# Optimization experiments

Hardware: AMD Instinct MI355X
Metric: run time of the kernel (lower is better)

## Reference

```python
import jax, jax.numpy as jnp
import numpy as np

EPS = 1e-5

def _ln(x, g, b):
    m = jnp.mean(x, -1, keepdims=True)
    v = jnp.var(x, -1, keepdims=True)
    return (x - m) / jnp.sqrt(v + EPS) * g + b

def _rel_shift(x):
    # x: [B, qlen, klen, n_head] -- TransformerXL relative shift
    b, q, k, n = x.shape
    xp = jnp.pad(x, ((0, 0), (0, 0), (1, 0), (0, 0)))  # zero-pad along klen front
    xp = xp.reshape(b, k + 1, q, n)[:, 1:]
    return xp.reshape(b, q, k, n)

def setup_inputs() -> dict:
    key = jax.random.key(0)
    B, Q, D, N, DH, DI = 4, 1024, 1024, 16, 64, 4096
    ks = jax.random.split(key, 9)
    s = 0.02
    w = jax.random.normal(ks[0], (B, Q, D), jnp.float32)
    r = jax.random.normal(ks[1], (1, Q, D), jnp.float32)
    attention_mask = jnp.triu(jnp.ones((Q, Q), bool), k=1)  # 1 == masked (causal)
    qkv_w = jax.random.normal(ks[2], (3 * D, D), jnp.float32) * s
    r_w = jax.random.normal(ks[3], (D, D), jnp.float32) * s
    o_w = jax.random.normal(ks[4], (D, D), jnp.float32) * s
    r_w_bias = jax.random.normal(ks[5], (N, DH), jnp.float32) * s
    r_r_bias = jax.random.normal(ks[6], (N, DH), jnp.float32) * s
    ln1_g = jnp.ones(D, jnp.float32); ln1_b = jnp.zeros(D, jnp.float32)
    ff_w1 = jax.random.normal(ks[7], (DI, D), jnp.float32) * s
    ff_b1 = jnp.zeros(DI, jnp.float32)
    ff_w2 = jax.random.normal(ks[8], (D, DI), jnp.float32) * s
    ff_b2 = jnp.zeros(D, jnp.float32)
    ln2_g = jnp.ones(D, jnp.float32); ln2_b = jnp.zeros(D, jnp.float32)
    return dict(w=w, r=r, attention_mask=attention_mask, qkv_w=qkv_w, r_w=r_w,
                o_w=o_w, r_w_bias=r_w_bias, r_r_bias=r_r_bias, ln1_g=ln1_g,
                ln1_b=ln1_b, ff_w1=ff_w1, ff_b1=ff_b1, ff_w2=ff_w2, ff_b2=ff_b2,
                ln2_g=ln2_g, ln2_b=ln2_b)

def reference(w, r, attention_mask, qkv_w, r_w, o_w, r_w_bias, r_r_bias,
              ln1_g, ln1_b, ff_w1, ff_b1, ff_w2, ff_b2, ln2_g, ln2_b):
    B, Q, D = w.shape
    N, DH = r_w_bias.shape
    # QKV projection (post-lnorm path, no mem)
    heads = w @ qkv_w.T  # [B,Q,3D]
    q, k, v = jnp.split(heads, 3, axis=-1)
    q = q.reshape(B, Q, N, DH)
    k = k.reshape(B, Q, N, DH)
    v = v.reshape(B, Q, N, DH)
    rk = (r[0] @ r_w.T).reshape(Q, N, DH)  # [rlen,N,DH]
    # content (AC) and position (BD) terms, computed in fp32 as in original
    AC = jnp.einsum('bind,bjnd->bijn', q + r_w_bias, k)
    BD = _rel_shift(jnp.einsum('bind,jnd->bijn', q + r_r_bias, rk))
    score = (AC + BD) * (1.0 / jnp.sqrt(jnp.float32(DH)))
    score = jnp.where(attention_mask[None, :, :, None], -1e30, score)
    prob = jax.nn.softmax(score, axis=2)  # softmax over klen
    av = jnp.einsum('bijn,bjnd->bind', prob, v).reshape(B, Q, D)
    out1 = _ln(w + av @ o_w.T, ln1_g, ln1_b)  # deepnorm_alpha = 1.0
    ff = jax.nn.relu(out1 @ ff_w1.T + ff_b1) @ ff_w2.T + ff_b2
    return _ln(out1 + ff, ln2_g, ln2_b)
```

## Files before the change

kernel.cpp:

```cpp
#include <hip/hip_runtime.h>
#include <hip/hip_bf16.h>

typedef __attribute__((ext_vector_type(8))) short short8;
typedef __attribute__((ext_vector_type(4))) short short4v;
typedef __attribute__((ext_vector_type(4))) float floatx4;

__device__ inline float bs2f(short s) {
    unsigned int u = ((unsigned int)(unsigned short)s) << 16;
    float f; __builtin_memcpy(&f, &u, 4); return f;
}
__device__ inline short f2bs(float f) {
    __hip_bfloat16 h = __float2bfloat16(f);
    unsigned short u; __builtin_memcpy(&u, &h, 2); return (short)u;
}
__device__ inline float ldf(const float* p)           { return *p; }
__device__ inline float ldf(const __hip_bfloat16* p)  { return __bfloat162float(*p); }
__device__ inline void  stf(float* p, float v)          { *p = v; }
__device__ inline void  stf(__hip_bfloat16* p, float v) { *p = __float2bfloat16(v); }

__device__ inline void gl_lds16(const short* g, short* l) {
    __builtin_amdgcn_global_load_lds(
        (const __attribute__((address_space(1))) void*)g,
        (__attribute__((address_space(3))) void*)l, 16, 0, 0);
}

__global__ __launch_bounds__(256) void f2b_all_kernel(
    const float* __restrict__ s0, const float* __restrict__ s1,
    const float* __restrict__ s2, const float* __restrict__ s3,
    const float* __restrict__ s4, const float* __restrict__ s5,
    const float* __restrict__ s6, __hip_bfloat16* __restrict__ dst)
{
    const long id  = blockIdx.x;
    const long gid = id * 1024 + threadIdx.x * 4;
    const float* src; long base;
    if      (id < 4096)  { src = s0; base = 0; }
    else if (id < 5120)  { src = s1; base = 4096L  * 1024; }
    else if (id < 8192)  { src = s2; base = 5120L  * 1024; }
    else if (id < 9216)  { src = s3; base = 8192L  * 1024; }
    else if (id < 10240) { src = s4; base = 9216L  * 1024; }
    else if (id < 14336) { src = s5; base = 10240L * 1024; }
    else                 { src = s6; base = 14336L * 1024; }
    const float4 v = *(const float4*)(src + (gid - base));
    dst[gid + 0] = __float2bfloat16(v.x);
    dst[gid + 1] = __float2bfloat16(v.y);
    dst[gid + 2] = __float2bfloat16(v.z);
    dst[gid + 3] = __float2bfloat16(v.w);
}

__global__ __launch_bounds__(256, 2) void gemm128_nt_kernel(
    const __hip_bfloat16* __restrict__ A,
    const __hip_bfloat16* __restrict__ Bw,
    __hip_bfloat16* __restrict__ C,
    int M, int N, int K,
    const float* __restrict__ bias,
    int do_relu)
{
    __shared__ short lA[128 * 32];
    __shared__ short lB[128 * 32];

    const int lane = threadIdx.x & 63;
    const int w    = threadIdx.x >> 6;
    const int m16  = lane & 15;
    const int quad = lane >> 4;
    const int wr   = w >> 1, wc = w & 1;

    const long i0 = (long)blockIdx.y * 128;
    const long j0 = (long)blockIdx.x * 128;

    const short* Ap = (const short*)A;
    const short* Bp = (const short*)Bw;

    floatx4 acc[4][4];
    #pragma unroll
    for (int a = 0; a < 4; ++a)
        #pragma unroll
        for (int b = 0; b < 4; ++b) acc[a][b] = (floatx4){0.f, 0.f, 0.f, 0.f};

    const int srow = w * 32 + (lane >> 2);
    const int scol = (lane & 3) * 8;
    const short* ga = Ap + (i0 + srow) * K + scol;
    const short* gb = Bp + (j0 + srow) * K + scol;
    short* la = lA + (w * 32) * 32;
    short* lb = lB + (w * 32) * 32;

    for (int k0 = 0; k0 < K; k0 += 32) {
        __syncthreads();
        gl_lds16(ga + k0,            la);
        gl_lds16(ga + 16 * K + k0,   la + 16 * 32);
        gl_lds16(gb + k0,            lb);
        gl_lds16(gb + 16 * K + k0,   lb + 16 * 32);
        __syncthreads();

        short8 af[4], bf[4];
        #pragma unroll
        for (int rb = 0; rb < 4; ++rb)
            af[rb] = *(const short8*)&lA[(wr * 64 + rb * 16 + m16) * 32 + quad * 8];
        #pragma unroll
        for (int cb = 0; cb < 4; ++cb)
            bf[cb] = *(const short8*)&lB[(wc * 64 + cb * 16 + m16) * 32 + quad * 8];
        #pragma unroll
        for (int rb = 0; rb < 4; ++rb)
            #pragma unroll
            for (int cb = 0; cb < 4; ++cb)
                acc[rb][cb] = __builtin_amdgcn_mfma_f32_16x16x32_bf16(
                    af[rb], bf[cb], acc[rb][cb], 0, 0, 0);
    }

    #pragma unroll
    for (int cb = 0; cb < 4; ++cb) {
        const long j = j0 + wc * 64 + cb * 16 + m16;
        const float bv = bias ? bias[j] : 0.f;
        #pragma unroll
        for (int rb = 0; rb < 4; ++rb) {
            #pragma unroll
            for (int rr = 0; rr < 4; ++rr) {
                const long row = i0 + wr * 64 + rb * 16 + quad * 4 + rr;
                float v = acc[rb][cb][rr] + bv;
                if (do_relu) v = fmaxf(v, 0.f);
                C[row * N + j] = __float2bfloat16(v);
            }
        }
    }
}

__global__ __launch_bounds__(256, 2) void gemm_n64_nt_kernel(
    const __hip_bfloat16* __restrict__ A,
    const __hip_bfloat16* __restrict__ Bw,
    __hip_bfloat16* __restrict__ C,
    int M, int N, int K,
    const float* __restrict__ bias,
    int do_relu)
{
    __shared__ short lA[128 * 32];
    __shared__ short lB[64 * 32];

    const int lane = threadIdx.x & 63;
    const int w    = threadIdx.x >> 6;
    const int m16  = lane & 15;
    const int quad = lane >> 4;
    const int wr   = w >> 1, wc = w & 1;

    const long i0 = (long)blockIdx.y * 128;
    const long j0 = (long)blockIdx.x * 64;

    const short* Ap = (const short*)A;
    const short* Bp = (const short*)Bw;

    floatx4 acc[4][2];
    #pragma unroll
    for (int a = 0; a < 4; ++a)
        #pragma unroll
        for (int b = 0; b < 2; ++b) acc[a][b] = (floatx4){0.f, 0.f, 0.f, 0.f};

    const int srowA = w * 32 + (lane >> 2);
    const int srowB = w * 16 + (lane >> 2);
    const int scol  = (lane & 3) * 8;
    const short* ga = Ap + (i0 + srowA) * K + scol;
    const short* gb = Bp + (j0 + srowB) * K + scol;
    short* la = lA + (w * 32) * 32;
    short* lb = lB + (w * 16) * 32;

    for (int k0 = 0; k0 < K; k0 += 32) {
        __syncthreads();
        gl_lds16(ga + k0,            la);
        gl_lds16(ga + 16 * K + k0,   la + 16 * 32);
        gl_lds16(gb + k0,            lb);
        __syncthreads();

        short8 af[4], bf[2];
        #pragma unroll
        for (int rb = 0; rb < 4; ++rb)
            af[rb] = *(const short8*)&lA[(wr * 64 + rb * 16 + m16) * 32 + quad * 8];
        #pragma unroll
        for (int cb = 0; cb < 2; ++cb)
            bf[cb] = *(const short8*)&lB[(wc * 32 + cb * 16 + m16) * 32 + quad * 8];
        #pragma unroll
        for (int rb = 0; rb < 4; ++rb)
            #pragma unroll
            for (int cb = 0; cb < 2; ++cb)
                acc[rb][cb] = __builtin_amdgcn_mfma_f32_16x16x32_bf16(
                    af[rb], bf[cb], acc[rb][cb], 0, 0, 0);
    }

    #pragma unroll
    for (int cb = 0; cb < 2; ++cb) {
        const long j = j0 + wc * 32 + cb * 16 + m16;
        const float bv = bias ? bias[j] : 0.f;
        #pragma unroll
        for (int rb = 0; rb < 4; ++rb) {
            #pragma unroll
            for (int rr = 0; rr < 4; ++rr) {
                const long row = i0 + wr * 64 + rb * 16 + quad * 4 + rr;
                float v = acc[rb][cb][rr] + bv;
                if (do_relu) v = fmaxf(v, 0.f);
                C[row * N + j] = __float2bfloat16(v);
            }
        }
    }
}

__global__ __launch_bounds__(256) void kvpack_kernel(
    const __hip_bfloat16* __restrict__ heads,
    short* __restrict__ kp, short* __restrict__ vp)
{
    const int Q = 1024, TD = 3072;
    __shared__ short kt[64 * 72];
    __shared__ short vt[64 * 72];
    const int tid = threadIdx.x;
    const int t  = blockIdx.x;
    const int bn = blockIdx.y;
    const int n = bn & 15, b = bn >> 4;
    const int j0 = t * 64;

    const short* hp = (const short*)heads + ((long)(b * Q + j0)) * TD + n * 64;
    {
        const int r = tid >> 2, c0 = (tid & 3) * 16;
        const short* src = hp + (long)r * TD + c0;
        *(short8*)&kt[r * 72 + c0]     = *(const short8*)(src + 1024);
        *(short8*)&kt[r * 72 + c0 + 8] = *(const short8*)(src + 1024 + 8);
        *(short8*)&vt[r * 72 + c0]     = *(const short8*)(src + 2048);
        *(short8*)&vt[r * 72 + c0 + 8] = *(const short8*)(src + 2048 + 8);
    }
    __syncthreads();

    const int lane = tid & 63;
    const int m16 = lane & 15, quad = lane >> 4;
    const long fb = ((long)bn * 16 + t) * 4096;
    #pragma unroll
    for (int pass = 0; pass < 2; ++pass) {
        const int fi = (tid >> 6) + pass * 4;
        const int c = fi >> 2, cb = fi & 3;
        short8 kf = *(const short8*)&kt[(cb * 16 + m16) * 72 + c * 32 + quad * 8];
        *(short8*)(kp + fb + fi * 512 + lane * 8) = kf;
        short8 vf;
        #pragma unroll
        for (int u = 0; u < 8; ++u)
            vf[u] = vt[(c * 32 + quad * 8 + u) * 72 + cb * 16 + m16];
        *(short8*)(vp + fb + fi * 512 + lane * 8) = vf;
    }
}

__global__ __launch_bounds__(256) void rkpack_kernel(
    const __hip_bfloat16* __restrict__ rkb, short* __restrict__ rkp)
{
    const int m = blockIdx.x;
    const int tid = threadIdx.x;
    const short4v v = *(const short4v*)((const short*)rkb + m * 1024 + tid * 4);
    const int n = tid >> 4, d = (tid * 4) & 63;
    *(short4v*)(rkp + ((long)n * 1024 + m) * 64 + d) = v;
}

__global__ __launch_bounds__(256, 2) void fattn_kernel(
    const __hip_bfloat16* __restrict__ heads,
    const short* __restrict__ kp,
    const short* __restrict__ vp,
    const short* __restrict__ rkp,
    const float* __restrict__ rwb,
    const float* __restrict__ rrb,
    __hip_bfloat16* __restrict__ av)
{
    const int Q = 1024, TD = 3072, D = 1024;
    const int tid  = threadIdx.x;
    const int lane = tid & 63;
    const int w    = tid >> 6;
    const int m16  = lane & 15;
    const int quad = lane >> 4;
    const int id = blockIdx.x;
    const int r8 = id & 7;
    const int z  = (id >> 3) & 7;
    const int bn = ((id >> 6) << 3) | r8;
    const int n = bn & 15, b = bn >> 4;

    __shared__ short pbuf[4][16 * 68];
    short* pb = pbuf[w];

    const short* hp = (const short*)heads;

    #pragma unroll
    for (int phase = 0; phase < 2; ++phase) {
        const int qt  = phase ? (15 - z) : z;
        const int iw0 = qt * 64 + w * 16;

        short8 qwf[2], qrf[2];
        {
            const long qoff = ((long)(b * Q + iw0 + m16)) * TD + n * 64;
            #pragma unroll
            for (int c = 0; c < 2; ++c) {
                short8 qv = *(const short8*)(hp + qoff + c * 32 + quad * 8);
                #pragma unroll
                for (int u = 0; u < 8; ++u) {
                    const int d = c * 32 + quad * 8 + u;
                    const float f = bs2f(qv[u]);
                    qwf[c][u] = f2bs(f + rwb[n * 64 + d]);
                    qrf[c][u] = f2bs(f + rrb[n * 64 + d]);
                }
            }
        }

        floatx4 oacc[4];
        #pragma unroll
        for (int t = 0; t < 4; ++t) oacc[t] = (floatx4){0.f, 0.f, 0.f, 0.f};
        float lsum[4] = {0.f, 0.f, 0.f, 0.f};

        for (int t = 0; t <= qt; ++t) {
            const int j0 = t * 64;
            const long fb = ((long)bn * 16 + t) * 4096 + lane * 8;

            short8 kf[8], vf[8];
            #pragma unroll
            for (int fi = 0; fi < 8; ++fi) {
                kf[fi] = *(const short8*)(kp + fb + fi * 512);
                vf[fi] = *(const short8*)(vp + fb + fi * 512);
            }
            short8 rf[5][2];
            const int m0 = Q - 16 + j0 - iw0;
            #pragma unroll
            for (int cb = 0; cb < 5; ++cb) {
                int m = m0 + cb * 16 + m16;
                if (m > Q - 1) m = Q - 1;
                const long roff = ((long)n * 1024 + m) * 64;
                #pragma unroll
                for (int c = 0; c < 2; ++c)
                    rf[cb][c] = *(const short8*)(rkp + roff + c * 32 + quad * 8);
            }

            floatx4 ac[4];
            #pragma unroll
            for (int cb = 0; cb < 4; ++cb) ac[cb] = (floatx4){0.f, 0.f, 0.f, 0.f};
            #pragma unroll
            for (int c = 0; c < 2; ++c)
                #pragma unroll
                for (int cb = 0; cb < 4; ++cb)
                    ac[cb] = __builtin_amdgcn_mfma_f32_16x16x32_bf16(
                        qwf[c], kf[c * 4 + cb], ac[cb], 0, 0, 0);

            floatx4 bd[5];
            #pragma unroll
            for (int cb = 0; cb < 5; ++cb) bd[cb] = (floatx4){0.f, 0.f, 0.f, 0.f};
            #pragma unroll
            for (int cb = 0; cb < 5; ++cb)
                #pragma unroll
                for (int c = 0; c < 2; ++c)
                    bd[cb] = __builtin_amdgcn_mfma_f32_16x16x32_bf16(
                        qrf[c], rf[cb][c], bd[cb], 0, 0, 0);

            #pragma unroll
            for (int r = 0; r < 4; ++r) {
                const int ii = quad * 4 + r;
                const int e  = 15 + m16 - ii;
                const int srcLane = (lane & 48) | (e & 15);
                float sh[5];
                #pragma unroll
                for (int cb = 0; cb < 5; ++cb)
                    sh[cb] = __shfl(bd[cb][r], srcLane, 64);
                #pragma unroll
                for (int cb = 0; cb < 4; ++cb) {
                    const float val = (e >= 16) ? sh[cb + 1] : sh[cb];
                    const float sc = (ac[cb][r] + val) * 0.125f;
                    const bool masked = (j0 + cb * 16 + m16) > (iw0 + ii);
                    const float p = masked ? 0.f : __expf(sc);
                    lsum[r] += p;
                    pb[ii * 68 + cb * 16 + m16] = f2bs(p);
                }
            }

            #pragma unroll
            for (int c = 0; c < 2; ++c) {
                const short* pp = pb + m16 * 68 + c * 32 + quad * 8;
                short4v plo = *(const short4v*)pp;
                short4v phi = *(const short4v*)(pp + 4);
                short8 pf;
                #pragma unroll
                for (int u = 0; u < 4; ++u) { pf[u] = plo[u]; pf[u + 4] = phi[u]; }
                #pragma unroll
                for (int cb = 0; cb < 4; ++cb)
                    oacc[cb] = __builtin_amdgcn_mfma_f32_16x16x32_bf16(
                        pf, vf[c * 4 + cb], oacc[cb], 0, 0, 0);
            }
        }

        #pragma unroll
        for (int r = 0; r < 4; ++r) {
            #pragma unroll
            for (int sft = 1; sft < 16; sft <<= 1)
                lsum[r] += __shfl_xor(lsum[r], sft, 64);
        }
        #pragma unroll
        for (int r = 0; r < 4; ++r) {
            const float linv = 1.f / lsum[r];
            #pragma unroll
            for (int cb = 0; cb < 4; ++cb) {
                const long row = (long)b * Q + iw0 + quad * 4 + r;
                av[row * D + n * 64 + cb * 16 + m16] =
                    __float2bfloat16(oacc[cb][r] * linv);
            }
        }
    }
}

template <typename TA, typename TB, typename TO>
__global__ __launch_bounds__(256) void ln_kernel(
    const TA* __restrict__ xa,
    const TB* __restrict__ xb,
    const float* __restrict__ g,
    const float* __restrict__ beta,
    TO* __restrict__ out)
{
    const int D = 1024;
    const long row = blockIdx.x;
    const int tid = threadIdx.x;
    const TA* pa = xa + row * D;
    const TB* pb = xb + row * D;

    float x[4];
    float s = 0.f, s2 = 0.f;
    #pragma unroll
    for (int u = 0; u < 4; ++u) {
        const int c = tid + u * 256;
        const float v = ldf(pa + c) + ldf(pb + c);
        x[u] = v; s += v; s2 += v * v;
    }
    #pragma unroll
    for (int sft = 32; sft > 0; sft >>= 1) {
        s  += __shfl_xor(s,  sft, 64);
        s2 += __shfl_xor(s2, sft, 64);
    }
    __shared__ float red[8];
    const int wv = tid >> 6, lane = tid & 63;
    if (lane == 0) { red[wv] = s; red[wv + 4] = s2; }
    __syncthreads();
    s  = red[0] + red[1] + red[2] + red[3];
    s2 = red[4] + red[5] + red[6] + red[7];
    const float mean = s * (1.f / D);
    const float var  = s2 * (1.f / D) - mean * mean;
    const float rstd = rsqrtf(var + 1e-5f);
    #pragma unroll
    for (int u = 0; u < 4; ++u) {
        const int c = tid + u * 256;
        const float v = (x[u] - mean) * rstd * g[c] + beta[c];
        stf(out + row * D + c, v);
    }
}

extern "C" void kernel_launch(void* const* d_in, const int* in_sizes, int n_in,
                              void* d_out, int out_size, void* d_ws, size_t ws_size,
                              hipStream_t stream)
{
    const int B = 4, Q = 1024, D = 1024, N = 16, TD = 3072, DI = 4096;
    const int BQ = B * Q;

    const float* w     = (const float*)d_in[0];
    const float* r     = (const float*)d_in[1];
    const float* qkv_w = (const float*)d_in[3];
    const float* r_w   = (const float*)d_in[4];
    const float* o_w   = (const float*)d_in[5];
    const float* rwb   = (const float*)d_in[6];
    const float* rrb   = (const float*)d_in[7];
    const float* ln1g  = (const float*)d_in[8];
    const float* ln1b  = (const float*)d_in[9];
    const float* ffw1  = (const float*)d_in[10];
    const float* ffb1  = (const float*)d_in[11];
    const float* ffw2  = (const float*)d_in[12];
    const float* ffb2  = (const float*)d_in[13];
    const float* ln2g  = (const float*)d_in[14];
    const float* ln2b  = (const float*)d_in[15];
    float* out = (float*)d_out;

    __hip_bfloat16* wsb   = (__hip_bfloat16*)d_ws;
    __hip_bfloat16* heads = wsb;
    __hip_bfloat16* rkb   = heads + (long)BQ * TD;
    __hip_bfloat16* av    = rkb   + (long)Q * D;
    __hip_bfloat16* ffh   = wsb;
    __hip_bfloat16* oproj = av    + (long)BQ * D;
    __hip_bfloat16* ff2o  = oproj;
    __hip_bfloat16* out1  = oproj + (long)BQ * D;
    __hip_bfloat16* cvt   = out1  + (long)BQ * D;
    __hip_bfloat16* wb    = cvt;
    __hip_bfloat16* rb    = wb    + (long)BQ * D;
    __hip_bfloat16* qkvwb = rb    + (long)Q * D;
    __hip_bfloat16* rwwb  = qkvwb + (long)TD * D;
    __hip_bfloat16* owb   = rwwb  + (long)D * D;
    __hip_bfloat16* f1wb  = owb   + (long)D * D;
    __hip_bfloat16* f2wb  = f1wb  + (long)DI * D;
    short* kp  = (short*)wb;
    short* vpk = (short*)rb;
    short* rkp = (short*)rwwb;

    const dim3 blk(256);

    f2b_all_kernel<<<dim3(18432), blk, 0, stream>>>(
        w, r, qkv_w, r_w, o_w, ffw1, ffw2, wb);

    gemm128_nt_kernel<<<dim3(TD / 128, BQ / 128), blk, 0, stream>>>(
        wb, qkvwb, heads, BQ, TD, D, nullptr, 0);
    gemm_n64_nt_kernel<<<dim3(D / 64, Q / 128), blk, 0, stream>>>(
        rb, rwwb, rkb, Q, D, D, nullptr, 0);
    kvpack_kernel<<<dim3(16, B * N), blk, 0, stream>>>(heads, kp, vpk);
    rkpack_kernel<<<dim3(Q), blk, 0, stream>>>(rkb, rkp);
    fattn_kernel<<<dim3(512), blk, 0, stream>>>(
        heads, kp, vpk, rkp, rwb, rrb, av);
    gemm_n64_nt_kernel<<<dim3(D / 64, BQ / 128), blk, 0, stream>>>(
        av, owb, oproj, BQ, D, D, nullptr, 0);
    ln_kernel<float, __hip_bfloat16, __hip_bfloat16>
        <<<dim3(BQ), blk, 0, stream>>>(w, oproj, ln1g, ln1b, out1);
    gemm128_nt_kernel<<<dim3(DI / 128, BQ / 128), blk, 0, stream>>>(
        out1, f1wb, ffh, BQ, DI, D, ffb1, 1);
    gemm_n64_nt_kernel<<<dim3(D / 64, BQ / 128), blk, 0, stream>>>(
        ffh, f2wb, ff2o, BQ, D, DI, ffb2, 0);
    ln_kernel<__hip_bfloat16, __hip_bfloat16, float>
        <<<dim3(BQ), blk, 0, stream>>>(out1, ff2o, ln2g, ln2b, out);
}
```

Measured before the change: 441.5 us.

## Split-K the N=1024 projections with LN-fused reduction; double-buffer K/V in attention

The output projection and FFN down-projection now use a 128x128 tile split-K GEMM with two K halves. Each half writes a bf16 partial, and a new three-input layernorm kernel sums both partials plus bias before normalising. The goal is better tile reuse and enough blocks to fill the GPU, since the 64-wide N tiles gave poor reuse. Separately, the attention loop double-buffers K/V fragments in registers so the next tile's loads overlap the current compute. This costs register pressure and extra partial-sum traffic, and rounding partials to bf16 adds precision loss.

```diff
diff --git a/kernel.cpp b/kernel.cpp
--- a/kernel.cpp
+++ b/kernel.cpp
@@ -123,6 +123,81 @@
     }
 }
 
+__global__ __launch_bounds__(256, 2) void gemm128_splitk_kernel(
+    const __hip_bfloat16* __restrict__ A,
+    const __hip_bfloat16* __restrict__ Bw,
+    __hip_bfloat16* __restrict__ C0,
+    __hip_bfloat16* __restrict__ C1,
+    int M, int N, int K)
+{
+    __shared__ short lA[128 * 32];
+    __shared__ short lB[128 * 32];
+
+    const int lane = threadIdx.x & 63;
+    const int w    = threadIdx.x >> 6;
+    const int m16  = lane & 15;
+    const int quad = lane >> 4;
+    const int wr   = w >> 1, wc = w & 1;
+
+    const long i0 = (long)blockIdx.y * 128;
+    const long j0 = (long)blockIdx.x * 128;
+    const int  kz = blockIdx.z;
+    const int  kbeg = kz * (K >> 1), kend = kbeg + (K >> 1);
+
+    const short* Ap = (const short*)A;
+    const short* Bp = (const short*)Bw;
+
+    floatx4 acc[4][4];
+    #pragma unroll
+    for (int a = 0; a < 4; ++a)
+        #pragma unroll
+        for (int b = 0; b < 4; ++b) acc[a][b] = (floatx4){0.f, 0.f, 0.f, 0.f};
+
+    const int srow = w * 32 + (lane >> 2);
+    const int scol = (lane & 3) * 8;
+    const short* ga = Ap + (i0 + srow) * K + scol;
+    const short* gb = Bp + (j0 + srow) * K + scol;
+    short* la = lA + (w * 32) * 32;
+    short* lb = lB + (w * 32) * 32;
+
+    for (int k0 = kbeg; k0 < kend; k0 += 32) {
+        __syncthreads();
+        gl_lds16(ga + k0,            la);
+        gl_lds16(ga + 16 * K + k0,   la + 16 * 32);
+        gl_lds16(gb + k0,            lb);
+        gl_lds16(gb + 16 * K + k0,   lb + 16 * 32);
+        __syncthreads();
+
+        short8 af[4], bf[4];
+        #pragma unroll
+        for (int rb = 0; rb < 4; ++rb)
+            af[rb] = *(const short8*)&lA[(wr * 64 + rb * 16 + m16) * 32 + quad * 8];
+        #pragma unroll
+        for (int cb = 0; cb < 4; ++cb)
+            bf[cb] = *(const short8*)&lB[(wc * 64 + cb * 16 + m16) * 32 + quad * 8];
+        #pragma unroll
+        for (int rb = 0; rb < 4; ++rb)
+            #pragma unroll
+            for (int cb = 0; cb < 4; ++cb)
+                acc[rb][cb] = __builtin_amdgcn_mfma_f32_16x16x32_bf16(
+                    af[rb], bf[cb], acc[rb][cb], 0, 0, 0);
+    }
+
+    __hip_bfloat16* C = kz ? C1 : C0;
+    #pragma unroll
+    for (int cb = 0; cb < 4; ++cb) {
+        const long j = j0 + wc * 64 + cb * 16 + m16;
+        #pragma unroll
+        for (int rb = 0; rb < 4; ++rb) {
+            #pragma unroll
+            for (int rr = 0; rr < 4; ++rr) {
+                const long row = i0 + wr * 64 + rb * 16 + quad * 4 + rr;
+                C[row * N + j] = __float2bfloat16(acc[rb][cb][rr]);
+            }
+        }
+    }
+}
+
 __global__ __launch_bounds__(256, 2) void gemm_n64_nt_kernel(
     const __hip_bfloat16* __restrict__ A,
     const __hip_bfloat16* __restrict__ Bw,
@@ -276,6 +351,8 @@
 
     const short* hp = (const short*)heads;
 
+    struct KV { short8 k[8], v[8]; };
+
     #pragma unroll
     for (int phase = 0; phase < 2; ++phase) {
         const int qt  = phase ? (15 - z) : z;
@@ -302,16 +379,18 @@
         for (int t = 0; t < 4; ++t) oacc[t] = (floatx4){0.f, 0.f, 0.f, 0.f};
         float lsum[4] = {0.f, 0.f, 0.f, 0.f};
 
-        for (int t = 0; t <= qt; ++t) {
+        auto loadKV = [&](KV& f, int t) {
+            const long fb = ((long)bn * 16 + t) * 4096 + lane * 8;
+            #pragma unroll
+            for (int fi = 0; fi < 8; ++fi) {
+                f.k[fi] = *(const short8*)(kp + fb + fi * 512);
+                f.v[fi] = *(const short8*)(vp + fb + fi * 512);
+            }
+        };
+
+        auto computeT = [&](const KV& f, int t) {
             const int j0 = t * 64;
-            const long fb = ((long)bn * 16 + t) * 4096 + lane * 8;
-
-            short8 kf[8], vf[8];
-            #pragma unroll
-            for (int fi = 0; fi < 8; ++fi) {
-                kf[fi] = *(const short8*)(kp + fb + fi * 512);
-                vf[fi] = *(const short8*)(vp + fb + fi * 512);
-            }
+
             short8 rf[5][2];
             const int m0 = Q - 16 + j0 - iw0;
             #pragma unroll
@@ -332,7 +411,7 @@
                 #pragma unroll
                 for (int cb = 0; cb < 4; ++cb)
                     ac[cb] = __builtin_amdgcn_mfma_f32_16x16x32_bf16(
-                        qwf[c], kf[c * 4 + cb], ac[cb], 0, 0, 0);
+                        qwf[c], f.k[c * 4 + cb], ac[cb], 0, 0, 0);
 
             floatx4 bd[5];
             #pragma unroll
@@ -375,8 +454,20 @@
                 #pragma unroll
                 for (int cb = 0; cb < 4; ++cb)
                     oacc[cb] = __builtin_amdgcn_mfma_f32_16x16x32_bf16(
-                        pf, vf[c * 4 + cb], oacc[cb], 0, 0, 0);
-            }
+                        pf, f.v[c * 4 + cb], oacc[cb], 0, 0, 0);
+            }
+        };
+
+        KV fa, fb;
+        loadKV(fa, 0);
+        int t = 0;
+        for (;;) {
+            if (t < qt) loadKV(fb, t + 1);
+            computeT(fa, t);
+            if (++t > qt) break;
+            if (t < qt) loadKV(fa, t + 1);
+            computeT(fb, t);
+            if (++t > qt) break;
         }
 
         #pragma unroll
@@ -418,6 +509,54 @@
     for (int u = 0; u < 4; ++u) {
         const int c = tid + u * 256;
         const float v = ldf(pa + c) + ldf(pb + c);
+        x[u] = v; s += v; s2 += v * v;
+    }
+    #pragma unroll
+    for (int sft = 32; sft > 0; sft >>= 1) {
+        s  += __shfl_xor(s,  sft, 64);
+        s2 += __shfl_xor(s2, sft, 64);
+    }
+    __shared__ float red[8];
+    const int wv = tid >> 6, lane = tid & 63;
+    if (lane == 0) { red[wv] = s; red[wv + 4] = s2; }
+    __syncthreads();
+    s  = red[0] + red[1] + red[2] + red[3];
+    s2 = red[4] + red[5] + red[6] + red[7];
+    const float mean = s * (1.f / D);
+    const float var  = s2 * (1.f / D) - mean * mean;
+    const float rstd = rsqrtf(var + 1e-5f);
+    #pragma unroll
+    for (int u = 0; u < 4; ++u) {
+        const int c = tid + u * 256;
+        const float v = (x[u] - mean) * rstd * g[c] + beta[c];
+        stf(out + row * D + c, v);
+    }
+}
+
+template <typename TA, typename TO>
+__global__ __launch_bounds__(256) void ln3_kernel(
+    const TA* __restrict__ xa,
+    const __hip_bfloat16* __restrict__ p0,
+    const __hip_bfloat16* __restrict__ p1,
+    const float* __restrict__ bias,
+    const float* __restrict__ g,
+    const float* __restrict__ beta,
+    TO* __restrict__ out)
+{
+    const int D = 1024;
+    const long row = blockIdx.x;
+    const int tid = threadIdx.x;
+    const TA* pa = xa + row * D;
+    const __hip_bfloat16* q0 = p0 + row * D;
+    const __hip_bfloat16* q1 = p1 + row * D;
+
+    float x[4];
+    float s = 0.f, s2 = 0.f;
+    #pragma unroll
+    for (int u = 0; u < 4; ++u) {
+        const int c = tid + u * 256;
+        float v = ldf(pa + c) + ldf(q0 + c) + ldf(q1 + c);
+        if (bias) v += bias[c];
         x[u] = v; s += v; s2 += v * v;
     }
     #pragma unroll
@@ -472,7 +611,6 @@
     __hip_bfloat16* av    = rkb   + (long)Q * D;
     __hip_bfloat16* ffh   = wsb;
     __hip_bfloat16* oproj = av    + (long)BQ * D;
-    __hip_bfloat16* ff2o  = oproj;
     __hip_bfloat16* out1  = oproj + (long)BQ * D;
     __hip_bfloat16* cvt   = out1  + (long)BQ * D;
     __hip_bfloat16* wb    = cvt;
@@ -485,6 +623,8 @@
     short* kp  = (short*)wb;
     short* vpk = (short*)rb;
     short* rkp = (short*)rwwb;
+    __hip_bfloat16* part0 = wb;
+    __hip_bfloat16* part1 = wb + (long)BQ * D;
 
     const dim3 blk(256);
 
@@ -499,14 +639,14 @@
     rkpack_kernel<<<dim3(Q), blk, 0, stream>>>(rkb, rkp);
     fattn_kernel<<<dim3(512), blk, 0, stream>>>(
         heads, kp, vpk, rkp, rwb, rrb, av);
-    gemm_n64_nt_kernel<<<dim3(D / 64, BQ / 128), blk, 0, stream>>>(
-        av, owb, oproj, BQ, D, D, nullptr, 0);
-    ln_kernel<float, __hip_bfloat16, __hip_bfloat16>
-        <<<dim3(BQ), blk, 0, stream>>>(w, oproj, ln1g, ln1b, out1);
+    gemm128_splitk_kernel<<<dim3(D / 128, BQ / 128, 2), blk, 0, stream>>>(
+        av, owb, part0, part1, BQ, D, D);
+    ln3_kernel<float, __hip_bfloat16>
+        <<<dim3(BQ), blk, 0, stream>>>(w, part0, part1, nullptr, ln1g, ln1b, out1);
     gemm128_nt_kernel<<<dim3(DI / 128, BQ / 128), blk, 0, stream>>>(
         out1, f1wb, ffh, BQ, DI, D, ffb1, 1);
-    gemm_n64_nt_kernel<<<dim3(D / 64, BQ / 128), blk, 0, stream>>>(
-        ffh, f2wb, ff2o, BQ, D, DI, ffb2, 0);
-    ln_kernel<__hip_bfloat16, __hip_bfloat16, float>
-        <<<dim3(BQ), blk, 0, stream>>>(out1, ff2o, ln2g, ln2b, out);
-}
+    gemm128_splitk_kernel<<<dim3(D / 128, BQ / 128, 2), blk, 0, stream>>>(
+        ffh, f2wb, part0, part1, BQ, D, DI);
+    ln3_kernel<__hip_bfloat16, float>
+        <<<dim3(BQ), blk, 0, stream>>>(out1, part0, part1, ffb2, ln2g, ln2b, out);
+}
```

Measured after the change: 395.7 us. 10.4% less time.
